# Kernel tuning notes

Hardware: AMD Instinct MI355X
Metric: run time of the kernel (lower is better)

## Reference

```python
import jax, jax.numpy as jnp
import numpy as np

VOCAB, EMB, H1, H2, T, B = 21, 128, 64, 100, 500, 1024


def lstm(x, W_ih, W_hh, b_ih, b_hh):
    # x: [B, T, D]; torch gate order i, f, g, o
    Bx, H = x.shape[0], W_hh.shape[1]
    xproj = jnp.einsum('btd,gd->btg', x, W_ih) + b_ih  # [B, T, 4H]

    def step(carry, xt):
        h, c = carry
        gates = xt + h @ W_hh.T + b_hh
        i, f, g, o = jnp.split(gates, 4, axis=-1)
        c = jax.nn.sigmoid(f) * c + jax.nn.sigmoid(i) * jnp.tanh(g)
        h = jax.nn.sigmoid(o) * jnp.tanh(c)
        return (h, c), h

    h0 = jnp.zeros((Bx, H), x.dtype)
    _, hs = jax.lax.scan(step, (h0, h0), xproj.transpose(1, 0, 2))
    return hs.transpose(1, 0, 2)  # [B, T, H]


def setup_inputs() -> dict:
    key = jax.random.key(0)
    ks = jax.random.split(key, 12)
    s = 0.05
    x_idx = jax.random.randint(ks[0], (B, T), 0, VOCAB, dtype=jnp.int32)
    emb_table = jax.random.normal(ks[1], (VOCAB, EMB), jnp.float32) * s
    emb_table = emb_table.at[0].set(0.0)  # padding_idx=0
    d = dict(
        x_idx=x_idx,
        emb_table=emb_table,
        W_ih1=jax.random.normal(ks[2], (4 * H1, EMB), jnp.float32) * s,
        W_hh1=jax.random.normal(ks[3], (4 * H1, H1), jnp.float32) * s,
        b_ih1=jax.random.normal(ks[4], (4 * H1,), jnp.float32) * s,
        b_hh1=jax.random.normal(ks[5], (4 * H1,), jnp.float32) * s,
        W_ih2=jax.random.normal(ks[6], (4 * H2, H1), jnp.float32) * s,
        W_hh2=jax.random.normal(ks[7], (4 * H2, H2), jnp.float32) * s,
        b_ih2=jax.random.normal(ks[8], (4 * H2,), jnp.float32) * s,
        b_hh2=jax.random.normal(ks[9], (4 * H2,), jnp.float32) * s,
        fc_w=jax.random.normal(ks[10], (1, H2), jnp.float32) * s,
        fc_b=jax.random.normal(ks[11], (1,), jnp.float32) * s,
    )
    return d


def reference(x_idx, emb_table, W_ih1, W_hh1, b_ih1, b_hh1,
              W_ih2, W_hh2, b_ih2, b_hh2, fc_w, fc_b):
    # embedding with padding_idx=0 (row is zero; mask keeps grads faithful)
    x = emb_table[x_idx] * (x_idx != 0)[..., None].astype(emb_table.dtype)  # [B,T,128]
    x = lstm(x, W_ih1, W_hh1, b_ih1, b_hh1)  # [B,T,64]
    # MaxPool1d(kernel=5, stride=5) over time
    Bx, Tx, D = x.shape
    Tp = Tx // 5
    x = x[:, :Tp * 5].reshape(Bx, Tp, 5, D).max(axis=2)  # [B,T/5,64]
    x = lstm(x, W_ih2, W_hh2, b_ih2, b_hh2)  # [B,T/5,100]
    h = x[:, -1, :]
    return jax.nn.sigmoid(h @ fc_w.T + fc_b)  # [B,1]
```

## Files before the change

kernel.cpp:

```cpp
#include <hip/hip_runtime.h>

#define VOCAB 21
#define EMB 128
#define H1 64
#define H2 100
#define T1 500
#define TP 100
#define NB 1024
#define TBL_LD 260
#define LOG2E 1.44269504f

typedef __attribute__((ext_vector_type(8))) short bf16x8;
typedef __attribute__((ext_vector_type(4))) float f32x4;

__device__ __forceinline__ unsigned short f2bf(float x){
    union { float f; unsigned u; } v; v.f = x;
    return (unsigned short)((v.u + 0x8000u) >> 16);
}
__device__ __forceinline__ void bar_lds(){
    asm volatile("s_waitcnt lgkmcnt(0)\n\ts_barrier" ::: "memory");
}
__device__ __forceinline__ float ex2(float x){ return __builtin_amdgcn_exp2f(x); }
__device__ __forceinline__ float rcp(float x){ return __builtin_amdgcn_rcpf(x); }

__global__ void k_table(const float* __restrict__ Wih, const float* __restrict__ emb,
                        const float* __restrict__ bih, const float* __restrict__ bhh,
                        float* __restrict__ table){
    const int p = threadIdx.x;
    const int v = blockIdx.x;
    const int orig = (p & 3) * H1 + (p >> 2);
    float s = bih[orig] + bhh[orig];
    if (v != 0){
        const float* w = Wih + orig * EMB;
        const float* e = emb + v * EMB;
        #pragma unroll 16
        for (int d = 0; d < EMB; ++d) s += w[d]*e[d];
    }
    table[v*TBL_LD + p] = s * LOG2E;
}

__global__ __launch_bounds__(1024, 1) void k_fused(
    const int* __restrict__ xidx, const float* __restrict__ Whh1,
    const float* __restrict__ tbl_g,
    const float* __restrict__ Wih2, const float* __restrict__ Whh2,
    const float* __restrict__ bih2, const float* __restrict__ bhh2,
    const float* __restrict__ fcw, const float* __restrict__ fcb,
    float* __restrict__ out){
  __shared__ __align__(16) float table[VOCAB*TBL_LD];
  __shared__ __align__(16) unsigned short hbuf[2][16*64];
  __shared__ __align__(16) unsigned short pool[2][16*64];
  __shared__ __align__(16) unsigned short h2buf[2][16*128];
  __shared__ int idxs[16*T1];
  __shared__ float fcred[16][16];

  const int tid = threadIdx.x;
  const int gt = tid >> 6, l = tid & 63;
  const int b0 = blockIdx.x * 16;
  const int row = l & 15, kg = l >> 4;

  for (int i = tid; i < VOCAB*TBL_LD; i += 1024) table[i] = tbl_g[i];
  for (int i = tid; i < 16*T1; i += 1024){
      int r = i / T1, t = i - r*T1;
      idxs[i] = xidx[(b0 + r)*T1 + t];
  }
  { unsigned short* hz = (unsigned short*)hbuf;
    for (int i = tid; i < 2048; i += 1024) hz[i] = 0; }
  { unsigned short* hz = (unsigned short*)h2buf;
    for (int i = tid; i < 4096; i += 1024) hz[i] = 0; }

  bf16x8 af0, af1;
  {
      const int p = 16*gt + row;
      const int orig = (p & 3)*H1 + (p >> 2);
      bf16x8 f;
      const float* s0 = Whh1 + orig*H1 + kg*8;
      #pragma unroll
      for (int j = 0; j < 8; ++j) f[j] = (short)f2bf(s0[j] * LOG2E);
      af0 = f;
      const float* s1 = Whh1 + orig*H1 + 32 + kg*8;
      #pragma unroll
      for (int j = 0; j < 8; ++j) f[j] = (short)f2bf(s1[j] * LOG2E);
      af1 = f;
  }

  const int nt2  = (gt < 10) ? 2 : 1;
  const int t2lo = (gt < 10) ? 2*gt : gt + 10;

  bf16x8 af2[2][6];
  #pragma unroll
  for (int u = 0; u < 2; ++u){
      if (u < nt2){
          const int p = 16*(t2lo + u) + row;
          const int cell_ = p >> 2, gate = p & 3;
          #pragma unroll
          for (int c = 0; c < 6; ++c){
              bf16x8 f;
              #pragma unroll
              for (int jj = 0; jj < 8; ++jj){
                  int k = c*32 + kg*8 + jj;
                  float vv = 0.f;
                  if (cell_ < H2){
                      if (k < 64)           vv = Wih2[(gate*H2 + cell_)*H1 + k];
                      else if (k < 64 + H2) vv = Whh2[(gate*H2 + cell_)*H2 + (k - 64)];
                  }
                  f[jj] = (short)f2bf(vv * LOG2E);
              }
              af2[u][c] = f;
          }
      }
  }

  f32x4 bz2[2];
  int cu2[2], wbh2[2];
  float fw2[2];
  const int swz = (row & 7) << 4;
  #pragma unroll
  for (int u = 0; u < 2; ++u){
      cu2[u] = 4*(t2lo + u) + kg;
      f32x4 b = {0.f,0.f,0.f,0.f};
      float fv = 0.f;
      if (u < nt2 && cu2[u] < H2){
          #pragma unroll
          for (int g = 0; g < 4; ++g)
              b[g] = (bih2[g*H2 + cu2[u]] + bhh2[g*H2 + cu2[u]]) * LOG2E;
          fv = fcw[cu2[u]];
      }
      bz2[u] = b; fw2[u] = fv;
      wbh2[u] = (row*256 + 2*cu2[u]) ^ swz;
  }
  const float twoL = 2.0f * LOG2E;

  char* hb  = (char*)hbuf;
  char* pb  = (char*)pool;
  char* h2b = (char*)h2buf;
  const int rb0  = (row*128 + 16*kg) ^ swz;
  const int rb1  = (row*128 + 64 + 16*kg) ^ swz;
  const int cell1 = 4*gt + kg;
  const int wbh1 = (row*128 + 2*cell1) ^ swz;
  int rbh2[4];
  #pragma unroll
  for (int j = 0; j < 4; ++j)
      rbh2[j] = (row*256 + 2*(j*32 + 8*kg)) ^ swz;

  float cc1 = 0.f, pm = -1e30f;
  float cc2[2] = {0.f, 0.f}, hv2[2] = {0.f, 0.f};
  __syncthreads();

  int vv = idxs[row*T1];
  f32x4 tq = *(const f32x4*)&table[vv*TBL_LD + 4*cell1];
  int vnext = idxs[row*T1 + 1];

  int rp1 = 0, rp2 = 0, t = 0;
  for (int tp = 0; tp < TP; ++tp){
      #pragma unroll
      for (int s = 0; s < 5; ++s, ++t){
          bf16x8 bf0 = *(const bf16x8*)(hb + rp1 + rb0);
          bf16x8 bf1 = *(const bf16x8*)(hb + rp1 + rb1);
          f32x4 a = __builtin_amdgcn_mfma_f32_16x16x32_bf16(af0, bf0, tq, 0,0,0);
          f32x4 z = __builtin_amdgcn_mfma_f32_16x16x32_bf16(af1, bf1, a, 0,0,0);
          f32x4 tqn = *(const f32x4*)&table[vnext*TBL_LD + 4*cell1];
          int vn2 = idxs[row*T1 + ((t + 2 < T1) ? (t + 2) : 0)];
          float si = rcp(1.f + ex2(-z[0]));
          float sf = rcp(1.f + ex2(-z[1]));
          float so = rcp(1.f + ex2(-z[3]));
          float tg = 1.f - 2.f*rcp(1.f + ex2(z[2] + z[2]));
          cc1 = sf*cc1 + si*tg;
          float th = 1.f - 2.f*rcp(1.f + ex2(twoL*cc1));
          float h = so*th;
          const int wp1 = rp1 ^ 2048;
          *(unsigned short*)(hb + wp1 + wbh1) = f2bf(h);
          pm = fmaxf(pm, h);
          if (s == 4){
              *(unsigned short*)(pb + ((tp & 1) ? 2048 : 0) + wbh1) = f2bf(pm);
              pm = -1e30f;
          }
          tq = tqn; vnext = vn2;
          rp1 = wp1;
          bar_lds();
      }
      {
          const int po = (tp & 1) ? 2048 : 0;
          bf16x8 x0 = *(const bf16x8*)(pb + po + rb0);
          bf16x8 x1 = *(const bf16x8*)(pb + po + rb1);
          bf16x8 h0 = *(const bf16x8*)(h2b + rp2 + rbh2[0]);
          bf16x8 h1 = *(const bf16x8*)(h2b + rp2 + rbh2[1]);
          bf16x8 h2 = *(const bf16x8*)(h2b + rp2 + rbh2[2]);
          bf16x8 h3 = *(const bf16x8*)(h2b + rp2 + rbh2[3]);
          const int wp2 = rp2 ^ 4096;
          #pragma unroll
          for (int u = 0; u < 2; ++u){
              if (u < nt2){
                  f32x4 za = __builtin_amdgcn_mfma_f32_16x16x32_bf16(af2[u][0], x0, bz2[u], 0,0,0);
                  f32x4 zb = __builtin_amdgcn_mfma_f32_16x16x32_bf16(af2[u][1], x1, (f32x4){0.f,0.f,0.f,0.f}, 0,0,0);
                  za = __builtin_amdgcn_mfma_f32_16x16x32_bf16(af2[u][2], h0, za, 0,0,0);
                  zb = __builtin_amdgcn_mfma_f32_16x16x32_bf16(af2[u][3], h1, zb, 0,0,0);
                  za = __builtin_amdgcn_mfma_f32_16x16x32_bf16(af2[u][4], h2, za, 0,0,0);
                  zb = __builtin_amdgcn_mfma_f32_16x16x32_bf16(af2[u][5], h3, zb, 0,0,0);
                  f32x4 q = za + zb;
                  float si = rcp(1.f + ex2(-q[0]));
                  float sf = rcp(1.f + ex2(-q[1]));
                  float so = rcp(1.f + ex2(-q[3]));
                  float tg = 1.f - 2.f*rcp(1.f + ex2(q[2] + q[2]));
                  cc2[u] = sf*cc2[u] + si*tg;
                  float th = 1.f - 2.f*rcp(1.f + ex2(twoL*cc2[u]));
                  hv2[u] = so*th;
                  if (cu2[u] < H2)
                      *(unsigned short*)(h2b + wp2 + wbh2[u]) = f2bf(hv2[u]);
              }
          }
          rp2 = wp2;
      }
  }

  float p = 0.f;
  #pragma unroll
  for (int u = 0; u < 2; ++u)
      if (u < nt2 && cu2[u] < H2) p += hv2[u] * fw2[u];
  p += __shfl_xor(p, 16);
  p += __shfl_xor(p, 32);
  if (l < 16) fcred[gt][l] = p;
  __syncthreads();
  if (tid < 16){
      float s = 0.f;
      #pragma unroll
      for (int ww = 0; ww < 16; ++ww) s += fcred[ww][tid];
      s += fcb[0];
      out[b0 + tid] = rcp(1.f + ex2(-s * LOG2E));
  }
}

extern "C" void kernel_launch(void* const* d_in, const int* in_sizes, int n_in,
                              void* d_out, int out_size, void* d_ws, size_t ws_size,
                              hipStream_t stream) {
    const int*   x_idx = (const int*)  d_in[0];
    const float* emb   = (const float*)d_in[1];
    const float* Wih1  = (const float*)d_in[2];
    const float* Whh1  = (const float*)d_in[3];
    const float* bih1  = (const float*)d_in[4];
    const float* bhh1  = (const float*)d_in[5];
    const float* Wih2  = (const float*)d_in[6];
    const float* Whh2  = (const float*)d_in[7];
    const float* bih2  = (const float*)d_in[8];
    const float* bhh2  = (const float*)d_in[9];
    const float* fcw   = (const float*)d_in[10];
    const float* fcb   = (const float*)d_in[11];
    float* out = (float*)d_out;

    float* table = (float*)d_ws;

    k_table<<<VOCAB, 256, 0, stream>>>(Wih1, emb, bih1, bhh1, table);
    k_fused<<<NB / 16, 1024, 0, stream>>>(x_idx, Whh1, table,
                                          Wih2, Whh2, bih2, bhh2,
                                          fcw, fcb, out);
}
```

Baseline: 289.3 us.

## Interleave layer-2 LSTM step across layer-1 substeps to hide its latency

The layer-2 LSTM step, which used to run as a separate block after every five layer-1 steps, is now split into stages spread over the five layer-1 substeps of the next pool window: operand loads, then three MFMA pairs, then gate math and writeback. This lags layer 2 by one pool window and adds an epilogue for the final step. The aim is to remove the serialized layer-2 critical path and overlap its MFMA and transcendental work with layer-1 latency, in exchange for more live registers and extra branching inside the unrolled loop. It relies on the double-buffered pool buffer still holding window tp-1 while layer 1 writes window tp.

```diff
diff --git a/kernel.cpp b/kernel.cpp
--- a/kernel.cpp
+++ b/kernel.cpp
@@ -144,6 +144,8 @@
 
   float cc1 = 0.f, pm = -1e30f;
   float cc2[2] = {0.f, 0.f}, hv2[2] = {0.f, 0.f};
+  bf16x8 x0 = {}, x1 = {}, h20 = {}, h21 = {}, h22 = {}, h23 = {};
+  f32x4 za[2], zb[2];
   __syncthreads();
 
   int vv = idxs[row*T1];
@@ -176,39 +178,79 @@
           }
           tq = tqn; vnext = vn2;
           rp1 = wp1;
-          bar_lds();
-      }
-      {
-          const int po = (tp & 1) ? 2048 : 0;
-          bf16x8 x0 = *(const bf16x8*)(pb + po + rb0);
-          bf16x8 x1 = *(const bf16x8*)(pb + po + rb1);
-          bf16x8 h0 = *(const bf16x8*)(h2b + rp2 + rbh2[0]);
-          bf16x8 h1 = *(const bf16x8*)(h2b + rp2 + rbh2[1]);
-          bf16x8 h2 = *(const bf16x8*)(h2b + rp2 + rbh2[2]);
-          bf16x8 h3 = *(const bf16x8*)(h2b + rp2 + rbh2[3]);
-          const int wp2 = rp2 ^ 4096;
-          #pragma unroll
-          for (int u = 0; u < 2; ++u){
-              if (u < nt2){
-                  f32x4 za = __builtin_amdgcn_mfma_f32_16x16x32_bf16(af2[u][0], x0, bz2[u], 0,0,0);
-                  f32x4 zb = __builtin_amdgcn_mfma_f32_16x16x32_bf16(af2[u][1], x1, (f32x4){0.f,0.f,0.f,0.f}, 0,0,0);
-                  za = __builtin_amdgcn_mfma_f32_16x16x32_bf16(af2[u][2], h0, za, 0,0,0);
-                  zb = __builtin_amdgcn_mfma_f32_16x16x32_bf16(af2[u][3], h1, zb, 0,0,0);
-                  za = __builtin_amdgcn_mfma_f32_16x16x32_bf16(af2[u][4], h2, za, 0,0,0);
-                  zb = __builtin_amdgcn_mfma_f32_16x16x32_bf16(af2[u][5], h3, zb, 0,0,0);
-                  f32x4 q = za + zb;
-                  float si = rcp(1.f + ex2(-q[0]));
-                  float sf = rcp(1.f + ex2(-q[1]));
-                  float so = rcp(1.f + ex2(-q[3]));
-                  float tg = 1.f - 2.f*rcp(1.f + ex2(q[2] + q[2]));
-                  cc2[u] = sf*cc2[u] + si*tg;
-                  float th = 1.f - 2.f*rcp(1.f + ex2(twoL*cc2[u]));
-                  hv2[u] = so*th;
-                  if (cu2[u] < H2)
-                      *(unsigned short*)(h2b + wp2 + wbh2[u]) = f2bf(hv2[u]);
+          if (tp > 0){
+              if (s == 0){
+                  const int po = ((tp - 1) & 1) ? 2048 : 0;
+                  x0  = *(const bf16x8*)(pb + po + rb0);
+                  x1  = *(const bf16x8*)(pb + po + rb1);
+                  h20 = *(const bf16x8*)(h2b + rp2 + rbh2[0]);
+                  h21 = *(const bf16x8*)(h2b + rp2 + rbh2[1]);
+                  h22 = *(const bf16x8*)(h2b + rp2 + rbh2[2]);
+                  h23 = *(const bf16x8*)(h2b + rp2 + rbh2[3]);
+              } else if (s == 1){
+                  #pragma unroll
+                  for (int u = 0; u < 2; ++u) if (u < nt2){
+                      za[u] = __builtin_amdgcn_mfma_f32_16x16x32_bf16(af2[u][0], x0, bz2[u], 0,0,0);
+                      zb[u] = __builtin_amdgcn_mfma_f32_16x16x32_bf16(af2[u][1], x1, (f32x4){0.f,0.f,0.f,0.f}, 0,0,0);
+                  }
+              } else if (s == 2){
+                  #pragma unroll
+                  for (int u = 0; u < 2; ++u) if (u < nt2){
+                      za[u] = __builtin_amdgcn_mfma_f32_16x16x32_bf16(af2[u][2], h20, za[u], 0,0,0);
+                      zb[u] = __builtin_amdgcn_mfma_f32_16x16x32_bf16(af2[u][3], h21, zb[u], 0,0,0);
+                  }
+              } else if (s == 3){
+                  #pragma unroll
+                  for (int u = 0; u < 2; ++u) if (u < nt2){
+                      za[u] = __builtin_amdgcn_mfma_f32_16x16x32_bf16(af2[u][4], h22, za[u], 0,0,0);
+                      zb[u] = __builtin_amdgcn_mfma_f32_16x16x32_bf16(af2[u][5], h23, zb[u], 0,0,0);
+                  }
+              } else {
+                  const int wp2 = rp2 ^ 4096;
+                  #pragma unroll
+                  for (int u = 0; u < 2; ++u) if (u < nt2){
+                      f32x4 q = za[u] + zb[u];
+                      float si2 = rcp(1.f + ex2(-q[0]));
+                      float sf2 = rcp(1.f + ex2(-q[1]));
+                      float so2 = rcp(1.f + ex2(-q[3]));
+                      float tg2 = 1.f - 2.f*rcp(1.f + ex2(q[2] + q[2]));
+                      cc2[u] = sf2*cc2[u] + si2*tg2;
+                      float th2 = 1.f - 2.f*rcp(1.f + ex2(twoL*cc2[u]));
+                      hv2[u] = so2*th2;
+                      if (cu2[u] < H2)
+                          *(unsigned short*)(h2b + wp2 + wbh2[u]) = f2bf(hv2[u]);
+                  }
+                  rp2 = wp2;
               }
           }
-          rp2 = wp2;
+          bar_lds();
+      }
+  }
+
+  {
+      const int po = (99 & 1) ? 2048 : 0;
+      x0  = *(const bf16x8*)(pb + po + rb0);
+      x1  = *(const bf16x8*)(pb + po + rb1);
+      h20 = *(const bf16x8*)(h2b + rp2 + rbh2[0]);
+      h21 = *(const bf16x8*)(h2b + rp2 + rbh2[1]);
+      h22 = *(const bf16x8*)(h2b + rp2 + rbh2[2]);
+      h23 = *(const bf16x8*)(h2b + rp2 + rbh2[3]);
+      #pragma unroll
+      for (int u = 0; u < 2; ++u) if (u < nt2){
+          f32x4 a1 = __builtin_amdgcn_mfma_f32_16x16x32_bf16(af2[u][0], x0, bz2[u], 0,0,0);
+          f32x4 b1 = __builtin_amdgcn_mfma_f32_16x16x32_bf16(af2[u][1], x1, (f32x4){0.f,0.f,0.f,0.f}, 0,0,0);
+          a1 = __builtin_amdgcn_mfma_f32_16x16x32_bf16(af2[u][2], h20, a1, 0,0,0);
+          b1 = __builtin_amdgcn_mfma_f32_16x16x32_bf16(af2[u][3], h21, b1, 0,0,0);
+          a1 = __builtin_amdgcn_mfma_f32_16x16x32_bf16(af2[u][4], h22, a1, 0,0,0);
+          b1 = __builtin_amdgcn_mfma_f32_16x16x32_bf16(af2[u][5], h23, b1, 0,0,0);
+          f32x4 q = a1 + b1;
+          float si2 = rcp(1.f + ex2(-q[0]));
+          float sf2 = rcp(1.f + ex2(-q[1]));
+          float so2 = rcp(1.f + ex2(-q[3]));
+          float tg2 = 1.f - 2.f*rcp(1.f + ex2(q[2] + q[2]));
+          cc2[u] = sf2*cc2[u] + si2*tg2;
+          float th2 = 1.f - 2.f*rcp(1.f + ex2(twoL*cc2[u]));
+          hv2[u] = so2*th2;
       }
   }
 
```

Result: slower. 325.3 us (+12.4%).
